# Kernel tuning notes

Hardware: AMD Instinct MI355X
Metric: run time of the kernel (lower is better)

Reference implementation:

```python
import jax, jax.numpy as jnp
import numpy as np

N, M, D, A = 10000, 32, 256, 128  # codes, max_ancestors(+self), embed dim, attention dim


def setup_inputs() -> dict:
    key = jax.random.key(0)
    k1, k2, k3, k4, k5 = jax.random.split(key, 5)
    basic_embeddings = jax.random.normal(k1, (N, D), jnp.float32) * 0.1
    # padded ancestry table; slot 0 is the code itself (diagonal filled in original)
    code_ancestry = jax.random.randint(k2, (N, M), 0, N)
    code_ancestry = code_ancestry.at[:, 0].set(jnp.arange(N))
    # variable-length valid prefix per code, like the original padding scheme
    lengths = jax.random.randint(k3, (N,), 1, M + 1)
    code_ancestry_mask = (jnp.arange(M)[None, :] < lengths[:, None]).astype(jnp.float32)
    Wp = jax.random.normal(k4, (A, 2 * D), jnp.float32) / np.float32(np.sqrt(2 * D))
    bp = jnp.zeros((A,), jnp.float32)
    Ww = jax.random.normal(k5, (1, A), jnp.float32) / np.float32(np.sqrt(A))
    return {
        "basic_embeddings": basic_embeddings,
        "code_ancestry": code_ancestry,
        "code_ancestry_mask": code_ancestry_mask,
        "Wp": Wp,
        "bp": bp,
        "Ww": Ww,
    }


def reference(basic_embeddings, code_ancestry, code_ancestry_mask, Wp, bp, Ww):
    # GRAM.ancestry_attention vmapped over all codes (compute_embeddings_mat with all-ones in_vec).
    d = basic_embeddings.shape[1]
    Wp_self, Wp_anc = Wp[:, :d], Wp[:, d:]  # hstack((e_i, e_j)) split: e_i part, ancestor part
    E = basic_embeddings[code_ancestry]  # [N, M, D] gathered ancestor embeddings
    # DAGAttention: weighted_sum(tanh(project(concat(e_i, e_j))))
    self_proj = basic_embeddings @ Wp_self.T              # [N, A]
    anc_proj = jnp.einsum('nmd,ad->nma', E, Wp_anc)       # [N, M, A]
    h = jnp.tanh(self_proj[:, None, :] + anc_proj + bp)   # [N, M, A]
    scores = jnp.einsum('nma,a->nm', h, Ww[0])            # [N, M]
    A_att = scores * code_ancestry_mask
    # unnormalized_softmax weights, then jnp.average over ancestors
    w = jnp.exp(A_att - jax.lax.stop_gradient(A_att.max(axis=-1, keepdims=True)))  # [N, M]
    G = jnp.einsum('nm,nmd->nd', w, E) / w.sum(axis=-1, keepdims=True)             # [N, D]
    return G
```

## Files before the change

### kernel.cpp

```cpp
#include <hip/hip_runtime.h>
#include <hip/hip_bf16.h>

#define NROW 10000
#define MANC 32
#define DIM  256
#define ADIM 128

typedef __attribute__((ext_vector_type(8))) short short8;
typedef __attribute__((ext_vector_type(4))) short short4v;
typedef __attribute__((ext_vector_type(4))) float floatx4;
typedef __attribute__((ext_vector_type(2))) unsigned int uint2v;

#if __has_builtin(__builtin_amdgcn_exp2f)
#define EXP2F(x) __builtin_amdgcn_exp2f(x)
#else
#define EXP2F(x) __expf((x) * 0.69314718055994531f)
#endif

#define C2L2E 2.8853900817779268f
#define L2E   1.4426950408889634f

static __device__ __forceinline__ short f2bf(float x) {
    union { __hip_bfloat16 h; short s; } u;
    u.h = __float2bfloat16(x);
    return u.s;
}
static __device__ __forceinline__ float bf2f(unsigned short u) {
    return __uint_as_float(((unsigned int)u) << 16);
}

__global__ __launch_bounds__(256) void proj_kernel(
    const float* __restrict__ be, const float* __restrict__ Wp,
    __hip_bfloat16* __restrict__ SP, __hip_bfloat16* __restrict__ beb) {
    __shared__ short lds[64 * 256];
    int q  = blockIdx.x & 3;
    int rb = blockIdx.x >> 2;
    int t  = threadIdx.x;

#pragma unroll
    for (int i = 0; i < 8; ++i) {
        int c  = i * 256 + t;
        int jl = c >> 5;
        int e0 = (c & 31) * 8;
        int j  = q * 64 + jl;
        const float* src = (j < ADIM) ? (Wp + (size_t)j * (2 * DIM) + e0)
                                      : (Wp + (size_t)(j - ADIM) * (2 * DIM) + DIM + e0);
        floatx4 v0 = *(const floatx4*)src;
        floatx4 v1 = *(const floatx4*)(src + 4);
        short8 s;
#pragma unroll
        for (int e = 0; e < 4; ++e) { s[e] = f2bf(v0[e]); s[4 + e] = f2bf(v1[e]); }
        int byte = (c * 16) ^ ((jl & 7) << 4);
        *(short8*)((char*)lds + byte) = s;
    }
    __syncthreads();

    int w    = t >> 6;
    int l    = t & 63;
    int tm   = rb * 4 + w;
    int arow = tm * 16 + (l & 15);
    int rcl  = min(arow, NROW - 1);
    int kc   = (l >> 4) * 8;
    const float* A = be + (size_t)rcl * DIM;

    floatx4 acc[4] = {{0,0,0,0},{0,0,0,0},{0,0,0,0},{0,0,0,0}};
#pragma unroll
    for (int k0 = 0; k0 < DIM; k0 += 32) {
        floatx4 a0 = *(const floatx4*)(A + k0 + kc);
        floatx4 a1 = *(const floatx4*)(A + k0 + kc + 4);
        short8 av;
#pragma unroll
        for (int e = 0; e < 4; ++e) { av[e] = f2bf(a0[e]); av[4 + e] = f2bf(a1[e]); }
        if (q == 0 && arow < NROW)
            *(short8*)((unsigned short*)beb + (size_t)arow * DIM + k0 + kc) = av;
#pragma unroll
        for (int tt = 0; tt < 4; ++tt) {
            int jl   = tt * 16 + (l & 15);
            int byte = (jl * 512 + (k0 + kc) * 2) ^ ((jl & 7) << 4);
            short8 bv = *(const short8*)((char*)lds + byte);
            acc[tt] = __builtin_amdgcn_mfma_f32_16x16x32_bf16(av, bv, acc[tt], 0, 0, 0);
        }
    }
    int orow = tm * 16 + ((l >> 4) << 2);
#pragma unroll
    for (int tt = 0; tt < 4; ++tt) {
#pragma unroll
        for (int r = 0; r < 4; ++r) {
            if (orow + r < NROW) {
                union { __hip_bfloat16 h; short s; } u;
                u.s = f2bf(acc[tt][r]);
                SP[(size_t)(orow + r) * DIM + q * 64 + tt * 16 + (l & 15)] = u.h;
            }
        }
    }
}

static __device__ __forceinline__ floatx4 score_tile(
    const unsigned short* __restrict__ SPu, int j, int kc,
    const float (&ssby)[4][8], const short8 (&bw)[4], floatx4 acc) {
    const unsigned short* p = SPu + (size_t)j * DIM + ADIM + kc;
#pragma unroll
    for (int kt = 0; kt < 4; ++kt) {
        short8 pv = *(const short8*)(p + kt * 32);
        short8 af;
#pragma unroll
        for (int i = 0; i < 8; ++i) {
            float y = fmaf(bf2f((unsigned short)pv[i]), C2L2E, ssby[kt][i]);
            y = __builtin_amdgcn_fmed3f(y, -28.f, 28.f);
            float e = EXP2F(y);
            float r = __builtin_amdgcn_rcpf(e + 1.f);
            af[i] = f2bf(fmaf(-2.f, r, 1.f));
        }
        acc = __builtin_amdgcn_mfma_f32_16x16x32_bf16(af, bw[kt], acc, 0, 0, 0);
    }
    return acc;
}

__global__ __launch_bounds__(256) void attn_kernel(
    const int*   __restrict__ anc,
    const float* __restrict__ mask,
    const float* __restrict__ bias,
    const float* __restrict__ Ww,
    const __hip_bfloat16* __restrict__ SP,
    const __hip_bfloat16* __restrict__ beb,
    float* __restrict__ out) {
    int tid = blockIdx.x * 256 + threadIdx.x;
    int l   = tid & 63;
    int n   = __builtin_amdgcn_readfirstlane(tid >> 6);
    int kc  = (l >> 4) * 8;
    const unsigned short* SPu = (const unsigned short*)SP;

    float ssby[4][8];
#pragma unroll
    for (int kt = 0; kt < 4; ++kt) {
        short8 sv = *(const short8*)(SPu + (size_t)n * DIM + kt * 32 + kc);
        floatx4 b0 = *(const floatx4*)(bias + kt * 32 + kc);
        floatx4 b1 = *(const floatx4*)(bias + kt * 32 + kc + 4);
#pragma unroll
        for (int i = 0; i < 8; ++i)
            ssby[kt][i] = (bf2f((unsigned short)sv[i]) + ((i < 4) ? b0[i & 3] : b1[i & 3])) * C2L2E;
    }

    float keep = ((l & 15) == 0) ? 1.f : 0.f;
    short8 bw[4];
#pragma unroll
    for (int kt = 0; kt < 4; ++kt) {
        floatx4 w0 = *(const floatx4*)(Ww + kt * 32 + kc);
        floatx4 w1 = *(const floatx4*)(Ww + kt * 32 + kc + 4);
#pragma unroll
        for (int i = 0; i < 8; ++i)
            bw[kt][i] = f2bf(((i < 4) ? w0[i & 3] : w1[i & 3]) * keep);
    }

    const int*   ancn = anc  + n * MANC;
    const float* mrow = mask + n * MANC;
    bool has2 = mrow[16] != 0.f;

    int m0 = l & 15;
    floatx4 acc0 = {0,0,0,0}, acc1 = {0,0,0,0};
    acc0 = score_tile(SPu, ancn[m0], kc, ssby, bw, acc0);
    if (has2)
        acc1 = score_tile(SPu, ancn[16 + m0], kc, ssby, bw, acc1);

    int rb = (l >> 4) << 2;
    float s0[4], s1[4];
#pragma unroll
    for (int r = 0; r < 4; ++r) {
        s0[r] = acc0[r] * mrow[rb + r];
        s1[r] = acc1[r] * mrow[16 + rb + r];
    }
    float mx = s0[0];
#pragma unroll
    for (int r = 0; r < 4; ++r) { mx = fmaxf(mx, s0[r]); mx = fmaxf(mx, s1[r]); }
    mx = fmaxf(mx, __shfl_xor(mx, 16, 64));
    mx = fmaxf(mx, __shfl_xor(mx, 32, 64));
    float nm = -mx * L2E;
    float wn0[4], wn1[4], tot = 0.f;
#pragma unroll
    for (int r = 0; r < 4; ++r) {
        wn0[r] = EXP2F(fmaf(s0[r], L2E, nm)); tot += wn0[r];
        wn1[r] = EXP2F(fmaf(s1[r], L2E, nm)); tot += wn1[r];
    }
    tot += __shfl_xor(tot, 16, 64);
    tot += __shfl_xor(tot, 32, 64);
    tot = __shfl(tot, 0, 64);
    float inv = __builtin_amdgcn_rcpf(tot);

    const unsigned short* ebase = (const unsigned short*)beb + (size_t)l * 4;
    float a0 = 0.f, a1 = 0.f, a2 = 0.f, a3 = 0.f;
#pragma unroll
    for (int m = 0; m < MANC; ++m) {
        int src = ((m & 15) >> 2) << 4;
        float wm = (m < 16) ? __shfl(wn0[m & 3], src, 64)
                            : __shfl(wn1[m & 3], src, 64);
        uint2v dv = *(const uint2v*)(ebase + (size_t)ancn[m] * DIM);
        a0 = fmaf(wm, __uint_as_float(dv.x << 16),          a0);
        a1 = fmaf(wm, __uint_as_float(dv.x & 0xffff0000u),  a1);
        a2 = fmaf(wm, __uint_as_float(dv.y << 16),          a2);
        a3 = fmaf(wm, __uint_as_float(dv.y & 0xffff0000u),  a3);
    }
    floatx4 res = {a0 * inv, a1 * inv, a2 * inv, a3 * inv};
    *(floatx4*)(out + (size_t)n * DIM + l * 4) = res;
}

extern "C" void kernel_launch(void* const* d_in, const int* in_sizes, int n_in,
                              void* d_out, int out_size, void* d_ws, size_t ws_size,
                              hipStream_t stream) {
    const float* be   = (const float*)d_in[0];
    const int*   anc  = (const int*)d_in[1];
    const float* mask = (const float*)d_in[2];
    const float* Wp   = (const float*)d_in[3];
    const float* bias = (const float*)d_in[4];
    const float* Ww   = (const float*)d_in[5];
    float* out = (float*)d_out;

    __hip_bfloat16* SPb = (__hip_bfloat16*)d_ws;
    __hip_bfloat16* beb = (__hip_bfloat16*)((char*)d_ws + (size_t)NROW * DIM * 2);

    proj_kernel<<<628, 256, 0, stream>>>(be, Wp, SPb, beb);
    attn_kernel<<<2500, 256, 0, stream>>>(anc, mask, bias, Ww, SPb, beb, out);
}
```

Baseline: 46.69 us.

## Split each code's attention across two wavefronts with LDS score exchange

The attention kernel now gives each code a 128-thread block of two wavefronts instead of one wavefront. Each wave scores 16 ancestors, the scores are exchanged through shared memory, and each wave gathers half of the embedding dimension. This is meant to halve the serial work per wave and raise parallelism, at the cost of duplicated setup, a block barrier, and four times as many blocks. The tanh input clamp is also removed, which saves one instruction per element but depends on exp2/rcp handling large arguments correctly.

```diff
diff --git a/kernel.cpp b/kernel.cpp
--- a/kernel.cpp
+++ b/kernel.cpp
@@ -7,9 +7,8 @@
 #define ADIM 128
 
 typedef __attribute__((ext_vector_type(8))) short short8;
-typedef __attribute__((ext_vector_type(4))) short short4v;
 typedef __attribute__((ext_vector_type(4))) float floatx4;
-typedef __attribute__((ext_vector_type(2))) unsigned int uint2v;
+typedef __attribute__((ext_vector_type(2))) float floatx2;
 
 #if __has_builtin(__builtin_amdgcn_exp2f)
 #define EXP2F(x) __builtin_amdgcn_exp2f(x)
@@ -106,7 +105,6 @@
 #pragma unroll
         for (int i = 0; i < 8; ++i) {
             float y = fmaf(bf2f((unsigned short)pv[i]), C2L2E, ssby[kt][i]);
-            y = __builtin_amdgcn_fmed3f(y, -28.f, 28.f);
             float e = EXP2F(y);
             float r = __builtin_amdgcn_rcpf(e + 1.f);
             af[i] = f2bf(fmaf(-2.f, r, 1.f));
@@ -116,7 +114,7 @@
     return acc;
 }
 
-__global__ __launch_bounds__(256) void attn_kernel(
+__global__ __launch_bounds__(128) void attn_kernel(
     const int*   __restrict__ anc,
     const float* __restrict__ mask,
     const float* __restrict__ bias,
@@ -124,10 +122,12 @@
     const __hip_bfloat16* __restrict__ SP,
     const __hip_bfloat16* __restrict__ beb,
     float* __restrict__ out) {
-    int tid = blockIdx.x * 256 + threadIdx.x;
-    int l   = tid & 63;
-    int n   = __builtin_amdgcn_readfirstlane(tid >> 6);
-    int kc  = (l >> 4) * 8;
+    __shared__ float sc[32];
+    int t  = threadIdx.x;
+    int l  = t & 63;
+    int h  = t >> 6;
+    int n  = blockIdx.x;
+    int kc = (l >> 4) * 8;
     const unsigned short* SPu = (const unsigned short*)SP;
 
     float ssby[4][8];
@@ -154,53 +154,48 @@
 
     const int*   ancn = anc  + n * MANC;
     const float* mrow = mask + n * MANC;
-    bool has2 = mrow[16] != 0.f;
-
-    int m0 = l & 15;
-    floatx4 acc0 = {0,0,0,0}, acc1 = {0,0,0,0};
-    acc0 = score_tile(SPu, ancn[m0], kc, ssby, bw, acc0);
-    if (has2)
-        acc1 = score_tile(SPu, ancn[16 + m0], kc, ssby, bw, acc1);
+    bool live = (h == 0) || (mrow[16] != 0.f);
 
     int rb = (l >> 4) << 2;
-    float s0[4], s1[4];
-#pragma unroll
-    for (int r = 0; r < 4; ++r) {
-        s0[r] = acc0[r] * mrow[rb + r];
-        s1[r] = acc1[r] * mrow[16 + rb + r];
-    }
-    float mx = s0[0];
-#pragma unroll
-    for (int r = 0; r < 4; ++r) { mx = fmaxf(mx, s0[r]); mx = fmaxf(mx, s1[r]); }
-    mx = fmaxf(mx, __shfl_xor(mx, 16, 64));
-    mx = fmaxf(mx, __shfl_xor(mx, 32, 64));
-    float nm = -mx * L2E;
-    float wn0[4], wn1[4], tot = 0.f;
-#pragma unroll
-    for (int r = 0; r < 4; ++r) {
-        wn0[r] = EXP2F(fmaf(s0[r], L2E, nm)); tot += wn0[r];
-        wn1[r] = EXP2F(fmaf(s1[r], L2E, nm)); tot += wn1[r];
-    }
-    tot += __shfl_xor(tot, 16, 64);
-    tot += __shfl_xor(tot, 32, 64);
-    tot = __shfl(tot, 0, 64);
-    float inv = __builtin_amdgcn_rcpf(tot);
-
-    const unsigned short* ebase = (const unsigned short*)beb + (size_t)l * 4;
-    float a0 = 0.f, a1 = 0.f, a2 = 0.f, a3 = 0.f;
+    float s0 = 0.f, s1 = 0.f, s2 = 0.f, s3 = 0.f;
+    if (live) {
+        int j = ancn[h * 16 + (l & 15)];
+        floatx4 acc = {0, 0, 0, 0};
+        acc = score_tile(SPu, j, kc, ssby, bw, acc);
+        s0 = acc[0] * mrow[h * 16 + rb + 0];
+        s1 = acc[1] * mrow[h * 16 + rb + 1];
+        s2 = acc[2] * mrow[h * 16 + rb + 2];
+        s3 = acc[3] * mrow[h * 16 + rb + 3];
+    }
+    if ((l & 15) == 0) {
+        floatx4 v = {s0, s1, s2, s3};
+        *(floatx4*)&sc[h * 16 + rb] = v;
+    }
+    __syncthreads();
+
+    float v = sc[l & 31];
+    float mx = v;
+#pragma unroll
+    for (int off = 1; off < 32; off <<= 1)
+        mx = fmaxf(mx, __shfl_xor(mx, off, 64));
+    float wgt = EXP2F((v - mx) * L2E);
+    float tot = wgt;
+#pragma unroll
+    for (int off = 1; off < 32; off <<= 1)
+        tot += __shfl_xor(tot, off, 64);
+    float wn = wgt * __builtin_amdgcn_rcpf(tot);
+
+    const unsigned short* ebase = (const unsigned short*)beb + h * 128 + l * 2;
+    float a0 = 0.f, a1 = 0.f;
 #pragma unroll
     for (int m = 0; m < MANC; ++m) {
-        int src = ((m & 15) >> 2) << 4;
-        float wm = (m < 16) ? __shfl(wn0[m & 3], src, 64)
-                            : __shfl(wn1[m & 3], src, 64);
-        uint2v dv = *(const uint2v*)(ebase + (size_t)ancn[m] * DIM);
-        a0 = fmaf(wm, __uint_as_float(dv.x << 16),          a0);
-        a1 = fmaf(wm, __uint_as_float(dv.x & 0xffff0000u),  a1);
-        a2 = fmaf(wm, __uint_as_float(dv.y << 16),          a2);
-        a3 = fmaf(wm, __uint_as_float(dv.y & 0xffff0000u),  a3);
-    }
-    floatx4 res = {a0 * inv, a1 * inv, a2 * inv, a3 * inv};
-    *(floatx4*)(out + (size_t)n * DIM + l * 4) = res;
+        float wm = __shfl(wn, m, 64);
+        unsigned int dv = *(const unsigned int*)(ebase + (size_t)ancn[m] * DIM);
+        a0 = fmaf(wm, __uint_as_float(dv << 16),         a0);
+        a1 = fmaf(wm, __uint_as_float(dv & 0xffff0000u), a1);
+    }
+    floatx2 res = {a0, a1};
+    *(floatx2*)(out + (size_t)n * DIM + h * 128 + l * 2) = res;
 }
 
 extern "C" void kernel_launch(void* const* d_in, const int* in_sizes, int n_in,
@@ -218,5 +213,5 @@
     __hip_bfloat16* beb = (__hip_bfloat16*)((char*)d_ws + (size_t)NROW * DIM * 2);
 
     proj_kernel<<<628, 256, 0, stream>>>(be, Wp, SPb, beb);
-    attn_kernel<<<2500, 256, 0, stream>>>(anc, mask, bias, Ww, SPb, beb, out);
-}
+    attn_kernel<<<10000, 128, 0, stream>>>(anc, mask, bias, Ww, SPb, beb, out);
+}
```

Result: slower. 49.60 us (+6.2%).
